# Kernel optimization log

Measured on AMD Instinct MI355X. Metric: run time of the kernel, lower is better.

The kernel has to match this reference:

```python
import jax, jax.numpy as jnp
import numpy as np

B, C, H, W = 16, 384, 64, 64
NUM_HEADS = 8
WINDOW = 8
GROUPS = 4
EPS = 1e-5


def setup_inputs() -> dict:
    key = jax.random.key(0)
    ks = jax.random.split(key, 6)
    x = jax.random.normal(ks[0], (B, C, H, W), dtype=jnp.float32)
    gn_weight = jnp.ones((C,), jnp.float32) + 0.02 * jax.random.normal(ks[1], (C,), jnp.float32)
    gn_bias = 0.02 * jax.random.normal(ks[2], (C,), jnp.float32)
    # torch nn.Linear weights: [out_features, in_features], y = x @ W.T
    w_qkv = jax.random.normal(ks[3], (3 * C, C), jnp.float32) / np.sqrt(C).astype(np.float32)
    w_proj = jax.random.normal(ks[4], (C, C), jnp.float32) / np.sqrt(C).astype(np.float32)
    b_proj = 0.01 * jax.random.normal(ks[5], (C,), jnp.float32)
    return {"x": x, "gn_weight": gn_weight, "gn_bias": gn_bias,
            "w_qkv": w_qkv, "w_proj": w_proj, "b_proj": b_proj}


def reference(x, gn_weight, gn_bias, w_qkv, w_proj, b_proj):
    Bb, Cc, Hh, Ww = x.shape
    ws, nh = WINDOW, NUM_HEADS
    hd = Cc // nh

    # GroupNorm(4, C) over NCHW
    xg = x.reshape(Bb, GROUPS, Cc // GROUPS, Hh, Ww)
    mean = xg.mean(axis=(2, 3, 4), keepdims=True)
    var = xg.var(axis=(2, 3, 4), keepdims=True)
    y = ((xg - mean) * jax.lax.rsqrt(var + EPS)).reshape(Bb, Cc, Hh, Ww)
    y = y * gn_weight[None, :, None, None] + gn_bias[None, :, None, None]

    # NCHW -> NHWC, pad to multiple of window
    y = y.transpose(0, 2, 3, 1)
    pad_h = (-Hh) % ws
    pad_w = (-Ww) % ws
    y = jnp.pad(y, ((0, 0), (0, pad_h), (0, pad_w), (0, 0)))
    Hp, Wp = Hh + pad_h, Ww + pad_w

    # window partition -> [Nw, S, C] with S = ws*ws
    win = y.reshape(Bb, Hp // ws, ws, Wp // ws, ws, Cc)
    win = win.transpose(0, 1, 3, 2, 4, 5).reshape(-1, ws * ws, Cc)
    Nw, S = win.shape[0], ws * ws

    # qkv projection (no bias)
    qkv = jnp.einsum('nsc,oc->nso', win, w_qkv)  # [Nw, S, 3C]
    qkv = qkv.reshape(Nw, S, 3, nh, hd).transpose(2, 0, 3, 1, 4)  # [3, Nw, nh, S, hd]
    q, k, v = qkv[0], qkv[1], qkv[2]

    scale = hd ** (-0.5)
    attn = jnp.einsum('nhqd,nhkd->nhqk', q * scale, k)
    attn = jax.nn.softmax(attn, axis=-1)
    h = jnp.einsum('nhqk,nhkd->nhqd', attn, v)  # [Nw, nh, S, hd]
    h = h.transpose(0, 2, 1, 3).reshape(Nw, S, Cc)

    # output projection
    h = jnp.einsum('nsc,oc->nso', h, w_proj) + b_proj

    # window unpartition, crop padding, NHWC -> NCHW, residual
    h = h.reshape(Bb, Hp // ws, Wp // ws, ws, ws, Cc)
    h = h.transpose(0, 1, 3, 2, 4, 5).reshape(Bb, Hp, Wp, Cc)
    h = h[:, :Hh, :Ww, :]
    return h.transpose(0, 3, 1, 2) + x
```

## Files before the change

### kernel.cpp

```cpp
#include <hip/hip_runtime.h>

#define BB 16
#define CC 384
#define HH 64
#define WWD 64
#define NH 8
#define HD 48
#define NW 1024
#define MTOK 65536
#define CPG 96
#define GSIZE (CPG*HH*WWD)

typedef __attribute__((ext_vector_type(8))) short short8;
typedef __attribute__((ext_vector_type(4))) short shortx4;
typedef __attribute__((ext_vector_type(4))) float floatx4;

static __device__ __forceinline__ float b2f(short s) {
    return __uint_as_float(((unsigned int)(unsigned short)s) << 16);
}
static __device__ __forceinline__ unsigned short f2b(float f) {
    unsigned int u = __float_as_uint(f);
    u = (u + 0x7FFF + ((u >> 16) & 1)) >> 16;
    return (unsigned short)u;
}

typedef __attribute__((address_space(1))) void gvoid;
typedef __attribute__((address_space(3))) void lvoid;
static __device__ __forceinline__ void gld16(const unsigned short* g, unsigned short* l) {
    __builtin_amdgcn_global_load_lds((gvoid*)(unsigned long long)g,
                                     (lvoid*)(unsigned int)(unsigned long long)l,
                                     16, 0, 0);
}

__global__ void gn_partial(const float* __restrict__ x, float* __restrict__ wsf) {
    int pair = blockIdx.x >> 3, slice = blockIdx.x & 7;
    const float4* p = (const float4*)(x + (size_t)pair * GSIZE + (size_t)slice * (GSIZE / 8));
    float s = 0.f, sq = 0.f;
    for (int i = threadIdx.x; i < GSIZE / 8 / 4; i += 256) {
        float4 v = p[i];
        s  += v.x + v.y + v.z + v.w;
        sq += v.x*v.x + v.y*v.y + v.z*v.z + v.w*v.w;
    }
    for (int o = 32; o; o >>= 1) { s += __shfl_down(s, o); sq += __shfl_down(sq, o); }
    __shared__ float ls[4], lq[4];
    int wv = threadIdx.x >> 6;
    if ((threadIdx.x & 63) == 0) { ls[wv] = s; lq[wv] = sq; }
    __syncthreads();
    if (threadIdx.x == 0) {
        s  = ls[0] + ls[1] + ls[2] + ls[3];
        sq = lq[0] + lq[1] + lq[2] + lq[3];
        wsf[pair * 8 + slice] = s;
        wsf[512 + pair * 8 + slice] = sq;
    }
}

__global__ void gn_final(float* wsf) {
    int p = threadIdx.x;
    float s = 0.f, sq = 0.f;
    for (int i = 0; i < 8; i++) { s += wsf[p * 8 + i]; sq += wsf[512 + p * 8 + i]; }
    float mean = s / (float)GSIZE;
    float var  = sq / (float)GSIZE - mean * mean;
    wsf[1024 + p] = mean;
    wsf[1088 + p] = rsqrtf(var + 1e-5f);
}

__global__ void norm_window(const float* __restrict__ x, const float* __restrict__ gamma,
                            const float* __restrict__ beta, const float* __restrict__ wsf,
                            unsigned short* __restrict__ win) {
    int nw = blockIdx.x;
    int b = nw >> 6, wh = (nw >> 3) & 7, ww = nw & 7;
    __shared__ float tile[CPG][66];
    int t = threadIdx.x;
    for (int g = 0; g < 4; g++) {
        float mean = wsf[1024 + b * 4 + g];
        float rstd = wsf[1088 + b * 4 + g];
        #pragma unroll
        for (int rr = 0; rr < 3; rr++) {
            int ridx = rr * 256 + t;
            int cl = ridx >> 3, i = ridx & 7;
            int cg = g * CPG + cl;
            const float* src = x + (((size_t)b * CC + cg) * HH + wh * 8 + i) * WWD + ww * 8;
            float ga = gamma[cg], be = beta[cg];
            float4 v0 = *(const float4*)src;
            float4 v1 = *(const float4*)(src + 4);
            float* dst = &tile[cl][i * 8];
            dst[0] = (v0.x - mean) * rstd * ga + be;
            dst[1] = (v0.y - mean) * rstd * ga + be;
            dst[2] = (v0.z - mean) * rstd * ga + be;
            dst[3] = (v0.w - mean) * rstd * ga + be;
            dst[4] = (v1.x - mean) * rstd * ga + be;
            dst[5] = (v1.y - mean) * rstd * ga + be;
            dst[6] = (v1.z - mean) * rstd * ga + be;
            dst[7] = (v1.w - mean) * rstd * ga + be;
        }
        __syncthreads();
        #pragma unroll
        for (int it = 0; it < 24; it++) {
            int idx = it * 256 + t;
            int cl = idx % 96, s = idx / 96;
            win[((size_t)nw * 64 + s) * CC + g * CPG + cl] = f2b(tile[cl][s]);
        }
        __syncthreads();
    }
}

__global__ void conv_w(const float* __restrict__ wqkv, const float* __restrict__ wproj,
                       unsigned short* __restrict__ wq_b, unsigned short* __restrict__ wp_b) {
    const int n1 = 1152 * 384, n2 = 384 * 384;
    const float qscale = 0.14433756729740643f;
    for (int i = blockIdx.x * 256 + threadIdx.x; i < n1 + n2; i += gridDim.x * 256) {
        if (i < n1) {
            float v = wqkv[i];
            if (i < 384 * 384) v *= qscale;
            wq_b[i] = f2b(v);
        } else {
            wp_b[i - n1] = f2b(wproj[i - n1]);
        }
    }
}

__launch_bounds__(256)
__global__ void gemm_qkv(const unsigned short* __restrict__ A, const unsigned short* __restrict__ Wb,
                         unsigned short* __restrict__ out) {
    const int K = 384, N = 1152;
    __shared__ unsigned short As[128 * 32], Bs[128 * 32];
    int m0 = blockIdx.y * 128, n0 = blockIdx.x * 128;
    int t = threadIdx.x;
    int lane = t & 63, wv = t >> 6;
    int wm = wv >> 1, wn = wv & 1;
    int quad = lane >> 4, l16 = lane & 15;
    int sr = lane >> 2, sc = (lane & 3) * 8;
    floatx4 acc[4][4] = {};
    for (int k0 = 0; k0 < K; k0 += 32) {
        const unsigned short* ga = A  + (size_t)(m0 + wv * 32 + sr) * K + k0 + sc;
        const unsigned short* gb = Wb + (size_t)(n0 + wv * 32 + sr) * K + k0 + sc;
        gld16(ga,            &As[wv * 1024]);
        gld16(ga + 16 * K,   &As[wv * 1024 + 512]);
        gld16(gb,            &Bs[wv * 1024]);
        gld16(gb + 16 * K,   &Bs[wv * 1024 + 512]);
        __syncthreads();
        short8 af[4], bf[4];
        #pragma unroll
        for (int mi = 0; mi < 4; mi++)
            af[mi] = *(const short8*)&As[(wm * 64 + mi * 16 + l16) * 32 + quad * 8];
        #pragma unroll
        for (int ni = 0; ni < 4; ni++)
            bf[ni] = *(const short8*)&Bs[(wn * 64 + ni * 16 + l16) * 32 + quad * 8];
        #pragma unroll
        for (int mi = 0; mi < 4; mi++)
            #pragma unroll
            for (int ni = 0; ni < 4; ni++)
                acc[mi][ni] = __builtin_amdgcn_mfma_f32_16x16x32_bf16(af[mi], bf[ni], acc[mi][ni], 0, 0, 0);
        __syncthreads();
    }
    #pragma unroll
    for (int mi = 0; mi < 4; mi++)
        #pragma unroll
        for (int ni = 0; ni < 4; ni++) {
            int gm = m0 + wm * 64 + mi * 16 + quad * 4;
            int gn = n0 + wn * 64 + ni * 16 + l16;
            #pragma unroll
            for (int r = 0; r < 4; r++)
                out[(size_t)(gm + r) * N + gn] = f2b(acc[mi][ni][r]);
        }
}

__launch_bounds__(256)
__global__ void attn(const unsigned short* __restrict__ qkv, unsigned short* __restrict__ hwin) {
    __shared__ unsigned short Pl[4][64 * 72];
    __shared__ unsigned short Vt[4][48 * 72];
    int t = threadIdx.x;
    int wv = t >> 6, lane = t & 63;
    int gw = blockIdx.x * 4 + wv;
    int wid = gw >> 3, head = gw & 7;
    int quad = lane >> 4, l16 = lane & 15;
    const unsigned short* base = qkv + (size_t)wid * 64 * 1152 + head * 48;

    {
        const unsigned short* vrow = base + 768 + (size_t)lane * 1152;
        #pragma unroll
        for (int c4 = 0; c4 < 12; c4++) {
            shortx4 v = *(const shortx4*)(vrow + c4 * 4);
            Vt[wv][(c4 * 4 + 0) * 72 + lane] = (unsigned short)v.x;
            Vt[wv][(c4 * 4 + 1) * 72 + lane] = (unsigned short)v.y;
            Vt[wv][(c4 * 4 + 2) * 72 + lane] = (unsigned short)v.z;
            Vt[wv][(c4 * 4 + 3) * 72 + lane] = (unsigned short)v.w;
        }
    }

    floatx4 acc[4][4] = {};
    #pragma unroll
    for (int ks = 0; ks < 2; ks++) {
        short8 qf[4], kf[4];
        #pragma unroll
        for (int mi = 0; mi < 4; mi++)
            qf[mi] = *(const short8*)(base + (size_t)(mi * 16 + l16) * 1152 + ks * 32 + quad * 8);
        #pragma unroll
        for (int ni = 0; ni < 4; ni++) {
            if (ks == 1 && quad >= 2) kf[ni] = (short8){};
            else kf[ni] = *(const short8*)(base + 384 + (size_t)(ni * 16 + l16) * 1152 + ks * 32 + quad * 8);
        }
        #pragma unroll
        for (int mi = 0; mi < 4; mi++)
            #pragma unroll
            for (int ni = 0; ni < 4; ni++)
                acc[mi][ni] = __builtin_amdgcn_mfma_f32_16x16x32_bf16(qf[mi], kf[ni], acc[mi][ni], 0, 0, 0);
    }

    float mx[4][4], sm[4][4];
    #pragma unroll
    for (int mi = 0; mi < 4; mi++)
        #pragma unroll
        for (int r = 0; r < 4; r++) {
            float m = acc[mi][0][r];
            m = fmaxf(m, acc[mi][1][r]);
            m = fmaxf(m, acc[mi][2][r]);
            m = fmaxf(m, acc[mi][3][r]);
            mx[mi][r] = m;
        }
    #pragma unroll
    for (int mask = 1; mask < 16; mask <<= 1)
        #pragma unroll
        for (int mi = 0; mi < 4; mi++)
            #pragma unroll
            for (int r = 0; r < 4; r++)
                mx[mi][r] = fmaxf(mx[mi][r], __shfl_xor(mx[mi][r], mask));
    #pragma unroll
    for (int mi = 0; mi < 4; mi++)
        #pragma unroll
        for (int r = 0; r < 4; r++) {
            float s = 0.f;
            #pragma unroll
            for (int ni = 0; ni < 4; ni++) {
                float p = __expf(acc[mi][ni][r] - mx[mi][r]);
                acc[mi][ni][r] = p;
                s += p;
            }
            sm[mi][r] = s;
        }
    #pragma unroll
    for (int mask = 1; mask < 16; mask <<= 1)
        #pragma unroll
        for (int mi = 0; mi < 4; mi++)
            #pragma unroll
            for (int r = 0; r < 4; r++)
                sm[mi][r] += __shfl_xor(sm[mi][r], mask);

    #pragma unroll
    for (int mi = 0; mi < 4; mi++)
        #pragma unroll
        for (int r = 0; r < 4; r++) {
            float inv = 1.f / sm[mi][r];
            int row = mi * 16 + quad * 4 + r;
            #pragma unroll
            for (int ni = 0; ni < 4; ni++)
                Pl[wv][row * 72 + ni * 16 + l16] = f2b(acc[mi][ni][r] * inv);
        }

    floatx4 o[4][3] = {};
    #pragma unroll
    for (int ks = 0; ks < 2; ks++) {
        short8 pf[4], vf[3];
        #pragma unroll
        for (int mi = 0; mi < 4; mi++)
            pf[mi] = *(const short8*)&Pl[wv][(mi * 16 + l16) * 72 + ks * 32 + quad * 8];
        #pragma unroll
        for (int ni = 0; ni < 3; ni++)
            vf[ni] = *(const short8*)&Vt[wv][(ni * 16 + l16) * 72 + ks * 32 + quad * 8];
        #pragma unroll
        for (int mi = 0; mi < 4; mi++)
            #pragma unroll
            for (int ni = 0; ni < 3; ni++)
                o[mi][ni] = __builtin_amdgcn_mfma_f32_16x16x32_bf16(pf[mi], vf[ni], o[mi][ni], 0, 0, 0);
    }

    unsigned short* orow = hwin + (size_t)wid * 64 * 384 + head * 48;
    #pragma unroll
    for (int mi = 0; mi < 4; mi++)
        #pragma unroll
        for (int ni = 0; ni < 3; ni++)
            #pragma unroll
            for (int r = 0; r < 4; r++)
                orow[(size_t)(mi * 16 + quad * 4 + r) * 384 + ni * 16 + l16] = f2b(o[mi][ni][r]);
}

__launch_bounds__(256)
__global__ void gemm_proj(const unsigned short* __restrict__ A, const unsigned short* __restrict__ Wb,
                          const float* __restrict__ bias, const float* __restrict__ x,
                          float* __restrict__ out) {
    const int K = 384;
    __shared__ unsigned short As[128 * 32], Bs[128 * 32];
    int m0 = blockIdx.y * 128, n0 = blockIdx.x * 128;
    int t = threadIdx.x;
    int lane = t & 63, wv = t >> 6;
    int wm = wv >> 1, wn = wv & 1;
    int quad = lane >> 4, l16 = lane & 15;
    int sr = lane >> 2, sc = (lane & 3) * 8;
    floatx4 acc[4][4] = {};
    for (int k0 = 0; k0 < K; k0 += 32) {
        const unsigned short* ga = A  + (size_t)(m0 + wv * 32 + sr) * K + k0 + sc;
        const unsigned short* gb = Wb + (size_t)(n0 + wv * 32 + sr) * K + k0 + sc;
        gld16(ga,          &As[wv * 1024]);
        gld16(ga + 16 * K, &As[wv * 1024 + 512]);
        gld16(gb,          &Bs[wv * 1024]);
        gld16(gb + 16 * K, &Bs[wv * 1024 + 512]);
        __syncthreads();
        short8 af[4], bf[4];
        #pragma unroll
        for (int mi = 0; mi < 4; mi++)
            af[mi] = *(const short8*)&As[(wm * 64 + mi * 16 + l16) * 32 + quad * 8];
        #pragma unroll
        for (int ni = 0; ni < 4; ni++)
            bf[ni] = *(const short8*)&Bs[(wn * 64 + ni * 16 + l16) * 32 + quad * 8];
        #pragma unroll
        for (int mi = 0; mi < 4; mi++)
            #pragma unroll
            for (int ni = 0; ni < 4; ni++)
                acc[mi][ni] = __builtin_amdgcn_mfma_f32_16x16x32_bf16(af[mi], bf[ni], acc[mi][ni], 0, 0, 0);
        __syncthreads();
    }
    #pragma unroll
    for (int mi = 0; mi < 4; mi++)
        #pragma unroll
        for (int ni = 0; ni < 4; ni++) {
            int gm = m0 + wm * 64 + mi * 16 + quad * 4;
            int gn = n0 + wn * 64 + ni * 16 + l16;
            float bv = bias[gn];
            int nw = gm >> 6, s = gm & 63;
            int b = nw >> 6, wh = (nw >> 3) & 7, ww = nw & 7;
            int i = s >> 3, jb = s & 7;
            size_t o = (((size_t)b * CC + gn) * HH + wh * 8 + i) * WWD + ww * 8 + jb;
            float4 xv = *(const float4*)(x + o);
            float4 ov;
            ov.x = acc[mi][ni][0] + bv + xv.x;
            ov.y = acc[mi][ni][1] + bv + xv.y;
            ov.z = acc[mi][ni][2] + bv + xv.z;
            ov.w = acc[mi][ni][3] + bv + xv.w;
            *(float4*)(out + o) = ov;
        }
}

extern "C" void kernel_launch(void* const* d_in, const int* in_sizes, int n_in,
                              void* d_out, int out_size, void* d_ws, size_t ws_size,
                              hipStream_t stream) {
    const float* x     = (const float*)d_in[0];
    const float* gnw   = (const float*)d_in[1];
    const float* gnb   = (const float*)d_in[2];
    const float* wqkv  = (const float*)d_in[3];
    const float* wproj = (const float*)d_in[4];
    const float* bproj = (const float*)d_in[5];
    float* out = (float*)d_out;

    char* ws = (char*)d_ws;
    float* wsf = (float*)ws;
    const size_t OFF_WQ  = 8192;
    const size_t OFF_WP  = OFF_WQ + (size_t)1152 * 384 * 2;
    const size_t OFF_WIN = 2097152;
    const size_t OFF_QKV = OFF_WIN + (size_t)MTOK * CC * 2 + 2048;
    unsigned short* wq_b = (unsigned short*)(ws + OFF_WQ);
    unsigned short* wp_b = (unsigned short*)(ws + OFF_WP);
    unsigned short* win  = (unsigned short*)(ws + OFF_WIN);
    unsigned short* qkvb = (unsigned short*)(ws + OFF_QKV);
    unsigned short* hwin = win;

    gn_partial<<<512, 256, 0, stream>>>(x, wsf);
    conv_w<<<2304, 256, 0, stream>>>(wqkv, wproj, wq_b, wp_b);
    gn_final<<<1, 64, 0, stream>>>(wsf);
    norm_window<<<1024, 256, 0, stream>>>(x, gnw, gnb, wsf, win);
    dim3 g1(9, 512);
    gemm_qkv<<<g1, 256, 0, stream>>>(win, wq_b, qkvb);
    attn<<<2048, 256, 0, stream>>>(qkvb, hwin);
    dim3 g2(3, 512);
    gemm_proj<<<g2, 256, 0, stream>>>(hwin, wp_b, bproj, x, out);
}
```

Baseline: 504.1 us.

## Widen GEMM K-steps, remap blocks per XCD, and stage outputs through LDS

Measured after the change: 488.9 us. 3.0% less time.

```diff
diff --git a/kernel.cpp b/kernel.cpp
--- a/kernel.cpp
+++ b/kernel.cpp
@@ -123,46 +123,64 @@
 __global__ void gemm_qkv(const unsigned short* __restrict__ A, const unsigned short* __restrict__ Wb,
                          unsigned short* __restrict__ out) {
     const int K = 384, N = 1152;
-    __shared__ unsigned short As[128 * 32], Bs[128 * 32];
-    int m0 = blockIdx.y * 128, n0 = blockIdx.x * 128;
+    __shared__ __align__(16) unsigned short smem[128 * 136];
+    unsigned short* As = smem;
+    unsigned short* Bs = smem + 8192;
+    int l = blockIdx.x;
+    int xcd = l & 7, li = l >> 3;
+    int m0 = (xcd * 64 + li / 9) * 128, n0 = (li % 9) * 128;
     int t = threadIdx.x;
     int lane = t & 63, wv = t >> 6;
     int wm = wv >> 1, wn = wv & 1;
     int quad = lane >> 4, l16 = lane & 15;
     int sr = lane >> 2, sc = (lane & 3) * 8;
     floatx4 acc[4][4] = {};
-    for (int k0 = 0; k0 < K; k0 += 32) {
-        const unsigned short* ga = A  + (size_t)(m0 + wv * 32 + sr) * K + k0 + sc;
-        const unsigned short* gb = Wb + (size_t)(n0 + wv * 32 + sr) * K + k0 + sc;
-        gld16(ga,            &As[wv * 1024]);
-        gld16(ga + 16 * K,   &As[wv * 1024 + 512]);
-        gld16(gb,            &Bs[wv * 1024]);
-        gld16(gb + 16 * K,   &Bs[wv * 1024 + 512]);
-        __syncthreads();
-        short8 af[4], bf[4];
-        #pragma unroll
-        for (int mi = 0; mi < 4; mi++)
-            af[mi] = *(const short8*)&As[(wm * 64 + mi * 16 + l16) * 32 + quad * 8];
-        #pragma unroll
-        for (int ni = 0; ni < 4; ni++)
-            bf[ni] = *(const short8*)&Bs[(wn * 64 + ni * 16 + l16) * 32 + quad * 8];
-        #pragma unroll
-        for (int mi = 0; mi < 4; mi++)
+    for (int k0 = 0; k0 < K; k0 += 64) {
+        #pragma unroll
+        for (int p = 0; p < 2; p++)
+            #pragma unroll
+            for (int rh = 0; rh < 2; rh++) {
+                const unsigned short* ga = A  + (size_t)(m0 + wv * 32 + rh * 16 + sr) * K + k0 + p * 32 + sc;
+                const unsigned short* gb = Wb + (size_t)(n0 + wv * 32 + rh * 16 + sr) * K + k0 + p * 32 + sc;
+                gld16(ga, &As[p * 4096 + (wv * 32 + rh * 16) * 32]);
+                gld16(gb, &Bs[p * 4096 + (wv * 32 + rh * 16) * 32]);
+            }
+        __syncthreads();
+        #pragma unroll
+        for (int p = 0; p < 2; p++) {
+            short8 af[4], bf[4];
+            #pragma unroll
+            for (int mi = 0; mi < 4; mi++)
+                af[mi] = *(const short8*)&As[p * 4096 + (wm * 64 + mi * 16 + l16) * 32 + quad * 8];
             #pragma unroll
             for (int ni = 0; ni < 4; ni++)
-                acc[mi][ni] = __builtin_amdgcn_mfma_f32_16x16x32_bf16(af[mi], bf[ni], acc[mi][ni], 0, 0, 0);
+                bf[ni] = *(const short8*)&Bs[p * 4096 + (wn * 64 + ni * 16 + l16) * 32 + quad * 8];
+            #pragma unroll
+            for (int mi = 0; mi < 4; mi++)
+                #pragma unroll
+                for (int ni = 0; ni < 4; ni++)
+                    acc[mi][ni] = __builtin_amdgcn_mfma_f32_16x16x32_bf16(af[mi], bf[ni], acc[mi][ni], 0, 0, 0);
+        }
         __syncthreads();
     }
     #pragma unroll
     for (int mi = 0; mi < 4; mi++)
         #pragma unroll
         for (int ni = 0; ni < 4; ni++) {
-            int gm = m0 + wm * 64 + mi * 16 + quad * 4;
-            int gn = n0 + wn * 64 + ni * 16 + l16;
+            int row = wm * 64 + mi * 16 + quad * 4;
+            int col = wn * 64 + ni * 16 + l16;
             #pragma unroll
             for (int r = 0; r < 4; r++)
-                out[(size_t)(gm + r) * N + gn] = f2b(acc[mi][ni][r]);
-        }
+                smem[(row + r) * 136 + col] = f2b(acc[mi][ni][r]);
+        }
+    __syncthreads();
+    int srow = wv * 4 + quad;
+    #pragma unroll
+    for (int i2 = 0; i2 < 8; i2++) {
+        int row = srow + i2 * 16;
+        short8 vv = *(const short8*)&smem[row * 136 + l16 * 8];
+        *(short8*)&out[(size_t)(m0 + row) * N + n0 + l16 * 8] = vv;
+    }
 }
 
 __launch_bounds__(256)
@@ -179,12 +197,11 @@
     {
         const unsigned short* vrow = base + 768 + (size_t)lane * 1152;
         #pragma unroll
-        for (int c4 = 0; c4 < 12; c4++) {
-            shortx4 v = *(const shortx4*)(vrow + c4 * 4);
-            Vt[wv][(c4 * 4 + 0) * 72 + lane] = (unsigned short)v.x;
-            Vt[wv][(c4 * 4 + 1) * 72 + lane] = (unsigned short)v.y;
-            Vt[wv][(c4 * 4 + 2) * 72 + lane] = (unsigned short)v.z;
-            Vt[wv][(c4 * 4 + 3) * 72 + lane] = (unsigned short)v.w;
+        for (int c8 = 0; c8 < 6; c8++) {
+            short8 v = *(const short8*)(vrow + c8 * 8);
+            #pragma unroll
+            for (int j = 0; j < 8; j++)
+                Vt[wv][(c8 * 8 + j) * 72 + lane] = (unsigned short)v[j];
         }
     }
 
@@ -212,10 +229,7 @@
     for (int mi = 0; mi < 4; mi++)
         #pragma unroll
         for (int r = 0; r < 4; r++) {
-            float m = acc[mi][0][r];
-            m = fmaxf(m, acc[mi][1][r]);
-            m = fmaxf(m, acc[mi][2][r]);
-            m = fmaxf(m, acc[mi][3][r]);
+            float m = fmaxf(fmaxf(acc[mi][0][r], acc[mi][1][r]), fmaxf(acc[mi][2][r], acc[mi][3][r]));
             mx[mi][r] = m;
         }
     #pragma unroll
@@ -274,14 +288,19 @@
                 o[mi][ni] = __builtin_amdgcn_mfma_f32_16x16x32_bf16(pf[mi], vf[ni], o[mi][ni], 0, 0, 0);
     }
 
-    unsigned short* orow = hwin + (size_t)wid * 64 * 384 + head * 48;
     #pragma unroll
     for (int mi = 0; mi < 4; mi++)
         #pragma unroll
         for (int ni = 0; ni < 3; ni++)
             #pragma unroll
             for (int r = 0; r < 4; r++)
-                orow[(size_t)(mi * 16 + quad * 4 + r) * 384 + ni * 16 + l16] = f2b(o[mi][ni][r]);
+                Pl[wv][(mi * 16 + quad * 4 + r) * 72 + ni * 16 + l16] = f2b(o[mi][ni][r]);
+    unsigned short* hw = hwin + (size_t)wid * 64 * 384 + head * 48;
+    #pragma unroll
+    for (int i2 = 0; i2 < 6; i2++) {
+        short8 vv = *(const short8*)&Pl[wv][lane * 72 + i2 * 8];
+        *(short8*)&hw[(size_t)lane * 384 + i2 * 8] = vv;
+    }
 }
 
 __launch_bounds__(256)
@@ -289,34 +308,42 @@
                           const float* __restrict__ bias, const float* __restrict__ x,
                           float* __restrict__ out) {
     const int K = 384;
-    __shared__ unsigned short As[128 * 32], Bs[128 * 32];
-    int m0 = blockIdx.y * 128, n0 = blockIdx.x * 128;
+    __shared__ __align__(16) unsigned short As[8192], Bs[8192];
+    int l = blockIdx.x;
+    int xcd = l & 7, li = l >> 3;
+    int m0 = (xcd * 64 + li / 3) * 128, n0 = (li % 3) * 128;
     int t = threadIdx.x;
     int lane = t & 63, wv = t >> 6;
     int wm = wv >> 1, wn = wv & 1;
     int quad = lane >> 4, l16 = lane & 15;
     int sr = lane >> 2, sc = (lane & 3) * 8;
     floatx4 acc[4][4] = {};
-    for (int k0 = 0; k0 < K; k0 += 32) {
-        const unsigned short* ga = A  + (size_t)(m0 + wv * 32 + sr) * K + k0 + sc;
-        const unsigned short* gb = Wb + (size_t)(n0 + wv * 32 + sr) * K + k0 + sc;
-        gld16(ga,          &As[wv * 1024]);
-        gld16(ga + 16 * K, &As[wv * 1024 + 512]);
-        gld16(gb,          &Bs[wv * 1024]);
-        gld16(gb + 16 * K, &Bs[wv * 1024 + 512]);
-        __syncthreads();
-        short8 af[4], bf[4];
-        #pragma unroll
-        for (int mi = 0; mi < 4; mi++)
-            af[mi] = *(const short8*)&As[(wm * 64 + mi * 16 + l16) * 32 + quad * 8];
-        #pragma unroll
-        for (int ni = 0; ni < 4; ni++)
-            bf[ni] = *(const short8*)&Bs[(wn * 64 + ni * 16 + l16) * 32 + quad * 8];
-        #pragma unroll
-        for (int mi = 0; mi < 4; mi++)
+    for (int k0 = 0; k0 < K; k0 += 64) {
+        #pragma unroll
+        for (int p = 0; p < 2; p++)
+            #pragma unroll
+            for (int rh = 0; rh < 2; rh++) {
+                const unsigned short* ga = A  + (size_t)(m0 + wv * 32 + rh * 16 + sr) * K + k0 + p * 32 + sc;
+                const unsigned short* gb = Wb + (size_t)(n0 + wv * 32 + rh * 16 + sr) * K + k0 + p * 32 + sc;
+                gld16(ga, &As[p * 4096 + (wv * 32 + rh * 16) * 32]);
+                gld16(gb, &Bs[p * 4096 + (wv * 32 + rh * 16) * 32]);
+            }
+        __syncthreads();
+        #pragma unroll
+        for (int p = 0; p < 2; p++) {
+            short8 af[4], bf[4];
+            #pragma unroll
+            for (int mi = 0; mi < 4; mi++)
+                af[mi] = *(const short8*)&As[p * 4096 + (wm * 64 + mi * 16 + l16) * 32 + quad * 8];
             #pragma unroll
             for (int ni = 0; ni < 4; ni++)
-                acc[mi][ni] = __builtin_amdgcn_mfma_f32_16x16x32_bf16(af[mi], bf[ni], acc[mi][ni], 0, 0, 0);
+                bf[ni] = *(const short8*)&Bs[p * 4096 + (wn * 64 + ni * 16 + l16) * 32 + quad * 8];
+            #pragma unroll
+            for (int mi = 0; mi < 4; mi++)
+                #pragma unroll
+                for (int ni = 0; ni < 4; ni++)
+                    acc[mi][ni] = __builtin_amdgcn_mfma_f32_16x16x32_bf16(af[mi], bf[ni], acc[mi][ni], 0, 0, 0);
+        }
         __syncthreads();
     }
     #pragma unroll
@@ -367,9 +394,7 @@
     conv_w<<<2304, 256, 0, stream>>>(wqkv, wproj, wq_b, wp_b);
     gn_final<<<1, 64, 0, stream>>>(wsf);
     norm_window<<<1024, 256, 0, stream>>>(x, gnw, gnb, wsf, win);
-    dim3 g1(9, 512);
-    gemm_qkv<<<g1, 256, 0, stream>>>(win, wq_b, qkvb);
+    gemm_qkv<<<4608, 256, 0, stream>>>(win, wq_b, qkvb);
     attn<<<2048, 256, 0, stream>>>(qkvb, hwin);
-    dim3 g2(3, 512);
-    gemm_proj<<<g2, 256, 0, stream>>>(hwin, wp_b, bproj, x, out);
-}
+    gemm_proj<<<1536, 256, 0, stream>>>(hwin, wp_b, bproj, x, out);
+}
```
